# Kernel tuning notes

Hardware: AMD Instinct MI355X
Metric: run time of the kernel (lower is better)

The kernel has to match this reference:

```python
import jax, jax.numpy as jnp
import numpy as np

B, S, L = 8, 2048, 8
H, NH = 768, 12
DH = H // NH
NUM_REL = 100
LN_EPS = 1e-5


def setup_inputs() -> dict:
    key = jax.random.key(0)
    ks = jax.random.split(key, 16)
    inp = {
        'text_embeddings': jax.random.normal(ks[0], (B, S, H), dtype=jnp.float32),
        # values in [-1, 64); -1 marks 'no leaf' and is masked out
        'graph_structure': jax.random.randint(ks[1], (B, S, L), -1, 64, dtype=jnp.int64),
        'relation_ids': jax.random.randint(ks[2], (B, S, L), 0, NUM_REL, dtype=jnp.int64),
        'rel_table': jax.random.normal(ks[3], (NUM_REL, H), dtype=jnp.float32),
        'Wq': jax.random.normal(ks[4], (H, H), dtype=jnp.float32) / np.sqrt(H),
        'bq': jnp.zeros((H,), dtype=jnp.float32),
        'Wk': jax.random.normal(ks[5], (H, H), dtype=jnp.float32) / np.sqrt(H),
        'bk': jnp.zeros((H,), dtype=jnp.float32),
        'Wv': jax.random.normal(ks[6], (H, H), dtype=jnp.float32) / np.sqrt(H),
        'bv': jnp.zeros((H,), dtype=jnp.float32),
        'Wo': jax.random.normal(ks[7], (H, H), dtype=jnp.float32) / np.sqrt(H),
        'bo': jnp.zeros((H,), dtype=jnp.float32),
        'gamma': jnp.ones((H,), dtype=jnp.float32),
        'beta': jnp.zeros((H,), dtype=jnp.float32),
    }
    return inp


def reference(text_embeddings, graph_structure, relation_ids, rel_table,
              Wq, bq, Wk, bk, Wv, bv, Wo, bo, gamma, beta):
    b, s, h = text_embeddings.shape
    l = relation_ids.shape[2]
    # embedding gather (clamp -1 -> 0, masked later)
    rel_emb = rel_table[jnp.clip(relation_ids, 0, None)]  # [B,S,L,H]
    # projections; query has length-1 per root token
    q = (text_embeddings @ Wq + bq).reshape(b, s, NH, DH)          # [B,S,N,D]
    k = (rel_emb @ Wk + bk).reshape(b, s, l, NH, DH)               # [B,S,L,N,D]
    v = (rel_emb @ Wv + bv).reshape(b, s, l, NH, DH)
    scores = jnp.einsum('bsnd,bslnd->bsnl', q, k) / np.sqrt(DH)    # [B,S,N,L]
    mask = (graph_structure != -1)[:, :, None, :]                  # [B,S,1,L]
    scores = jnp.where(mask, scores, jnp.float32(-10000.0))
    probs = jax.nn.softmax(scores, axis=-1)                        # [B,S,N,L]
    ctx = jnp.einsum('bsnl,bslnd->bsnd', probs, v).reshape(b, s, h)
    out = ctx @ Wo + bo
    x = text_embeddings + out
    mu = jnp.mean(x, axis=-1, keepdims=True)
    var = jnp.mean(jnp.square(x - mu), axis=-1, keepdims=True)
    return (x - mu) * jax.lax.rsqrt(var + LN_EPS) * gamma + beta
```

## Files before the change

### kernel.cpp

```cpp
#include <hip/hip_runtime.h>
#include <hip/hip_bf16.h>

#define H 768
#define NH 12
#define DH 64
#define LL 8
#define NTOK 16384
#define NREL 100
#define NRELP 128
#define PADW 72

typedef __attribute__((ext_vector_type(8))) short short8;
typedef __attribute__((ext_vector_type(4))) float f32x4;

__device__ __forceinline__ float bf2f(ushort u) {
  union { unsigned int i; float f; } v; v.i = ((unsigned int)u) << 16; return v.f;
}
__device__ __forceinline__ float bflo(unsigned int u) {
  union { unsigned int i; float f; } v; v.i = u << 16; return v.f;
}
__device__ __forceinline__ float bfhi(unsigned int u) {
  union { unsigned int i; float f; } v; v.i = u & 0xffff0000u; return v.f;
}
__device__ __forceinline__ ushort f2bf(float f) {
  union { float f; unsigned int i; } v; v.f = f;
  unsigned int x = v.i;
  return (ushort)((x + 0x7fffu + ((x >> 16) & 1u)) >> 16);
}

#define NBX 12288
#define NBR 96
__global__ __launch_bounds__(256) void cvt_all_kernel(
    const float* __restrict__ X, ushort* __restrict__ Xbf,
    const float* __restrict__ rel, ushort* __restrict__ RelB) {
  int b = blockIdx.x;
  if (b < NBX) {
    int i = (b * 256 + threadIdx.x) * 4;
    float4 v = *(const float4*)(X + i);
    ushort4 o; o.x = f2bf(v.x); o.y = f2bf(v.y); o.z = f2bf(v.z); o.w = f2bf(v.w);
    *(ushort4*)(Xbf + i) = o;
  } else {
    int i = ((b - NBX) * 256 + threadIdx.x) * 4;
    int row = i / H;
    ushort4 o = {0, 0, 0, 0};
    if (row < NREL) {
      float4 v = *(const float4*)(rel + i);
      o.x = f2bf(v.x); o.y = f2bf(v.y); o.z = f2bf(v.z); o.w = f2bf(v.w);
    }
    *(ushort4*)(RelB + i) = o;
  }
}

__global__ __launch_bounds__(256) void transpose4_kernel(
    const float* __restrict__ s0, ushort* __restrict__ d0,
    const float* __restrict__ s1, ushort* __restrict__ d1,
    const float* __restrict__ s2, ushort* __restrict__ d2,
    const float* __restrict__ s3, ushort* __restrict__ d3) {
  const float* src; ushort* dst;
  switch (blockIdx.z) {
    case 0:  src = s0; dst = d0; break;
    case 1:  src = s1; dst = d1; break;
    case 2:  src = s2; dst = d2; break;
    default: src = s3; dst = d3; break;
  }
  __shared__ float tile[32][33];
  int bx = blockIdx.x * 32, by = blockIdx.y * 32;
  int tx = threadIdx.x & 31, ty = threadIdx.x >> 5;
  #pragma unroll
  for (int i = 0; i < 32; i += 8)
    tile[ty + i][tx] = src[(size_t)(by + ty + i) * H + bx + tx];
  __syncthreads();
  #pragma unroll
  for (int i = 0; i < 32; i += 8)
    dst[(size_t)(bx + ty + i) * H + by + tx] = f2bf(tile[tx][ty + i]);
}

__device__ __forceinline__ void gload_lds16(const void* g, void* l) {
  __builtin_amdgcn_global_load_lds(
      (const __attribute__((address_space(1))) unsigned int*)g,
      (__attribute__((address_space(3))) unsigned int*)l, 16, 0, 0);
}

#define BM 128
#define BN 128
#define BK 64

__device__ __forceinline__ void gemm_body(
    const ushort* __restrict__ A,
    const ushort* __restrict__ Bt,
    const float* __restrict__ bias,
    ushort* __restrict__ C,
    int M, int N, int K, int bx, int by) {
  __shared__ ushort As[BM * BK];
  __shared__ ushort Bs[BN * BK];
  const int tid = threadIdx.x;
  const int row0 = by * BM;
  const int col0 = bx * BN;
  const int wave = tid >> 6;
  const int lane = tid & 63;
  const int wr = wave >> 1, wc = wave & 1;
  const int lr = lane & 15, lk = lane >> 4;
  f32x4 acc[4][4];
  #pragma unroll
  for (int m = 0; m < 4; ++m)
    #pragma unroll
    for (int n = 0; n < 4; ++n) acc[m][n] = (f32x4)(0.f);

  for (int k0 = 0; k0 < K; k0 += BK) {
    #pragma unroll
    for (int i = 0; i < 4; ++i) {
      int c = tid + i * 256;
      int r = c >> 3, s = c & 7;
      int gs = s ^ (r & 7);
      gload_lds16(A  + (size_t)(row0 + r) * K + k0 + gs * 8, (char*)As + c * 16);
      gload_lds16(Bt + (size_t)(col0 + r) * K + k0 + gs * 8, (char*)Bs + c * 16);
    }
    __syncthreads();
    #pragma unroll
    for (int kk = 0; kk < 2; ++kk) {
      const int sw = (((kk << 2) | lk) ^ (lr & 7)) * 8;
      short8 af[4], bfr[4];
      #pragma unroll
      for (int m = 0; m < 4; ++m)
        af[m] = *(const short8*)(As + (wr * 64 + m * 16 + lr) * BK + sw);
      #pragma unroll
      for (int n = 0; n < 4; ++n)
        bfr[n] = *(const short8*)(Bs + (wc * 64 + n * 16 + lr) * BK + sw);
      #pragma unroll
      for (int m = 0; m < 4; ++m)
        #pragma unroll
        for (int n = 0; n < 4; ++n)
          acc[m][n] = __builtin_amdgcn_mfma_f32_16x16x32_bf16(af[m], bfr[n], acc[m][n], 0, 0, 0);
    }
    __syncthreads();
  }
  #pragma unroll
  for (int m = 0; m < 4; ++m) {
    #pragma unroll
    for (int n = 0; n < 4; ++n) {
      int col = col0 + wc * 64 + n * 16 + lr;
      float b = bias[col];
      #pragma unroll
      for (int j = 0; j < 4; ++j) {
        int row = row0 + wr * 64 + m * 16 + lk * 4 + j;
        C[(size_t)row * N + col] = f2bf(acc[m][n][j] + b);
      }
    }
  }
}

__global__ __launch_bounds__(256, 2) void gemm_bt_kernel(
    const ushort* __restrict__ A, const ushort* __restrict__ Bt,
    const float* __restrict__ bias, ushort* __restrict__ C,
    int M, int N, int K) {
  int lin = blockIdx.y * gridDim.x + blockIdx.x;
  int q = (gridDim.x * gridDim.y) >> 3;
  int wg = (lin & 7) * q + (lin >> 3);
  gemm_body(A, Bt, bias, C, M, N, K, wg % gridDim.x, wg / gridDim.x);
}

__global__ __launch_bounds__(256, 2) void gemm_kv_kernel(
    const ushort* __restrict__ A,
    const ushort* __restrict__ BtK, const float* __restrict__ bK, ushort* __restrict__ CK,
    const ushort* __restrict__ BtV, const float* __restrict__ bV, ushort* __restrict__ CV) {
  if (blockIdx.z == 0)
    gemm_body(A, BtK, bK, CK, NRELP, H, H, blockIdx.x, blockIdx.y);
  else
    gemm_body(A, BtV, bV, CV, NRELP, H, H, blockIdx.x, blockIdx.y);
}

__global__ __launch_bounds__(256) void attn3_kernel(
    const ushort* __restrict__ Q,
    const ushort* __restrict__ Ktab,
    const ushort* __restrict__ Vtab,
    const int* __restrict__ graph,
    const int* __restrict__ relid,
    ushort* __restrict__ Ctx) {
  __shared__ __align__(16) ushort Ks[NREL * PADW];
  __shared__ __align__(16) ushort Vs[NREL * PADW];
  const int tid = threadIdx.x;
  const int head = blockIdx.y;
  const int t = blockIdx.x * 256 + tid;

  #pragma unroll
  for (int i = 0; i < 4; ++i) {
    int c = tid + i * 256;
    if (c < NREL * 9) {
      int row = c / 9, slot = c - row * 9;
      int gs = (slot < 8) ? slot * 8 : 0;
      const size_t src = (size_t)row * H + head * DH + gs;
      gload_lds16(Ktab + src, (char*)Ks + (size_t)c * 16);
      gload_lds16(Vtab + src, (char*)Vs + (size_t)c * 16);
    }
  }

  const uint4* qp = (const uint4*)(Q + (size_t)t * H + head * DH);
  uint4 qw[8];
  #pragma unroll
  for (int j = 0; j < 8; ++j) qw[j] = qp[j];
  const int4* gp = (const int4*)(graph + (size_t)t * LL);
  const int4* rp = (const int4*)(relid + (size_t)t * LL);
  int4 ga = gp[0], gb = gp[1];
  int4 ra = rp[0], rb = rp[1];
  int gs[8] = {ga.x, ga.y, ga.z, ga.w, gb.x, gb.y, gb.z, gb.w};
  int rid[8] = {ra.x, ra.y, ra.z, ra.w, rb.x, rb.y, rb.z, rb.w};
  int koff[8];
  #pragma unroll
  for (int l = 0; l < 8; ++l) {
    int r = rid[l] < 0 ? 0 : rid[l];
    koff[l] = r * (PADW * 2);
  }

  __syncthreads();

  float s[8];
  #pragma unroll
  for (int l = 0; l < 8; ++l) s[l] = 0.f;
  #pragma unroll
  for (int j = 0; j < 8; ++j) {
    float qf[8];
    qf[0] = bflo(qw[j].x); qf[1] = bfhi(qw[j].x);
    qf[2] = bflo(qw[j].y); qf[3] = bfhi(qw[j].y);
    qf[4] = bflo(qw[j].z); qf[5] = bfhi(qw[j].z);
    qf[6] = bflo(qw[j].w); qf[7] = bfhi(qw[j].w);
    #pragma unroll
    for (int l = 0; l < 8; ++l) {
      uint4 kw = *(const uint4*)((const char*)Ks + koff[l] + j * 16);
      s[l] += qf[0] * bflo(kw.x) + qf[1] * bfhi(kw.x)
            + qf[2] * bflo(kw.y) + qf[3] * bfhi(kw.y)
            + qf[4] * bflo(kw.z) + qf[5] * bfhi(kw.z)
            + qf[6] * bflo(kw.w) + qf[7] * bfhi(kw.w);
    }
  }

  #pragma unroll
  for (int l = 0; l < 8; ++l)
    s[l] = (gs[l] != -1) ? s[l] * 0.125f : -10000.0f;
  float mx = s[0];
  #pragma unroll
  for (int l = 1; l < 8; ++l) mx = fmaxf(mx, s[l]);
  float p[8], den = 0.f;
  #pragma unroll
  for (int l = 0; l < 8; ++l) { p[l] = __expf(s[l] - mx); den += p[l]; }
  float inv = 1.f / den;
  #pragma unroll
  for (int l = 0; l < 8; ++l) p[l] *= inv;

  ushort* cp = Ctx + (size_t)t * H + head * DH;
  #pragma unroll
  for (int j = 0; j < 8; ++j) {
    float a[8];
    #pragma unroll
    for (int d = 0; d < 8; ++d) a[d] = 0.f;
    #pragma unroll
    for (int l = 0; l < 8; ++l) {
      uint4 vw = *(const uint4*)((const char*)Vs + koff[l] + j * 16);
      a[0] += p[l] * bflo(vw.x); a[1] += p[l] * bfhi(vw.x);
      a[2] += p[l] * bflo(vw.y); a[3] += p[l] * bfhi(vw.y);
      a[4] += p[l] * bflo(vw.z); a[5] += p[l] * bfhi(vw.z);
      a[6] += p[l] * bflo(vw.w); a[7] += p[l] * bfhi(vw.w);
    }
    short8 o;
    #pragma unroll
    for (int d = 0; d < 8; ++d) o[d] = (short)f2bf(a[d]);
    *(short8*)(cp + j * 8) = o;
  }
}

__global__ __launch_bounds__(192) void ln_kernel(
    const float* __restrict__ text, const ushort* __restrict__ op,
    const float* __restrict__ gamma, const float* __restrict__ beta,
    float* __restrict__ out) {
  int t = blockIdx.x;
  int c0 = threadIdx.x * 4;
  float4 tv = *(const float4*)(text + (size_t)t * H + c0);
  ushort4 ov = *(const ushort4*)(op + (size_t)t * H + c0);
  float x0 = tv.x + bf2f(ov.x), x1 = tv.y + bf2f(ov.y);
  float x2 = tv.z + bf2f(ov.z), x3 = tv.w + bf2f(ov.w);
  float s = x0 + x1 + x2 + x3;
  float s2 = x0 * x0 + x1 * x1 + x2 * x2 + x3 * x3;
  #pragma unroll
  for (int off = 32; off > 0; off >>= 1) {
    s  += __shfl_xor(s, off, 64);
    s2 += __shfl_xor(s2, off, 64);
  }
  __shared__ float red[2][3];
  int wave = threadIdx.x >> 6, lane = threadIdx.x & 63;
  if (lane == 0) { red[0][wave] = s; red[1][wave] = s2; }
  __syncthreads();
  s  = red[0][0] + red[0][1] + red[0][2];
  s2 = red[1][0] + red[1][1] + red[1][2];
  float mu = s * (1.f / H);
  float var = s2 * (1.f / H) - mu * mu;
  float rs = rsqrtf(var + 1e-5f);
  float4 g4 = *(const float4*)(gamma + c0);
  float4 b4 = *(const float4*)(beta + c0);
  float4 o4;
  o4.x = (x0 - mu) * rs * g4.x + b4.x;
  o4.y = (x1 - mu) * rs * g4.y + b4.y;
  o4.z = (x2 - mu) * rs * g4.z + b4.z;
  o4.w = (x3 - mu) * rs * g4.w + b4.w;
  *(float4*)(out + (size_t)t * H + c0) = o4;
}

extern "C" void kernel_launch(void* const* d_in, const int* in_sizes, int n_in,
                              void* d_out, int out_size, void* d_ws, size_t ws_size,
                              hipStream_t stream) {
  const float* text      = (const float*)d_in[0];
  const int*   graph     = (const int*)d_in[1];
  const int*   relid     = (const int*)d_in[2];
  const float* rel_table = (const float*)d_in[3];
  const float* Wq = (const float*)d_in[4];  const float* bq = (const float*)d_in[5];
  const float* Wk = (const float*)d_in[6];  const float* bk = (const float*)d_in[7];
  const float* Wv = (const float*)d_in[8];  const float* bv = (const float*)d_in[9];
  const float* Wo = (const float*)d_in[10]; const float* bo = (const float*)d_in[11];
  const float* gamma = (const float*)d_in[12];
  const float* beta  = (const float*)d_in[13];
  float* out = (float*)d_out;
  char* ws = (char*)d_ws;

  const size_t TOKH = (size_t)NTOK * H;
  size_t off = 0;
  ushort* Xbf  = (ushort*)(ws + off); off += TOKH * 2;
  ushort* Qbf  = (ushort*)(ws + off); off += TOKH * 2;
  ushort* WqT  = (ushort*)(ws + off); off += (size_t)H * H * 2;
  ushort* WoT  = (ushort*)(ws + off); off += (size_t)H * H * 2;
  ushort* WkT  = (ushort*)(ws + off); off += (size_t)H * H * 2;
  ushort* WvT  = (ushort*)(ws + off); off += (size_t)H * H * 2;
  ushort* RelB = (ushort*)(ws + off); off += (size_t)NRELP * H * 2;
  ushort* Ktab = (ushort*)(ws + off); off += (size_t)NRELP * H * 2;
  ushort* Vtab = (ushort*)(ws + off); off += (size_t)NRELP * H * 2;

  cvt_all_kernel<<<NBX + NBR, 256, 0, stream>>>(text, Xbf, rel_table, RelB);
  transpose4_kernel<<<dim3(H / 32, H / 32, 4), 256, 0, stream>>>(
      Wq, WqT, Wo, WoT, Wk, WkT, Wv, WvT);
  gemm_kv_kernel<<<dim3(H / BN, NRELP / BM, 2), 256, 0, stream>>>(
      RelB, WkT, bk, Ktab, WvT, bv, Vtab);
  dim3 g1(H / BN, NTOK / BM);
  gemm_bt_kernel<<<g1, 256, 0, stream>>>(Xbf, WqT, bq, Qbf, NTOK, H, H);
  dim3 ga(NTOK / 256, NH);
  attn3_kernel<<<ga, 256, 0, stream>>>(Qbf, Ktab, Vtab, graph, relid, Xbf);
  gemm_bt_kernel<<<g1, 256, 0, stream>>>(Xbf, WoT, bo, Qbf, NTOK, H, H);
  ln_kernel<<<NTOK, 192, 0, stream>>>(text, Qbf, gamma, beta, out);
}
```

Measured before the change: 124.0 us.

## Fuse fp32-to-bf16 conversion into Q GEMM and merge prep launches

```diff
diff --git a/kernel.cpp b/kernel.cpp
--- a/kernel.cpp
+++ b/kernel.cpp
@@ -27,35 +27,32 @@
   unsigned int x = v.i;
   return (ushort)((x + 0x7fffu + ((x >> 16) & 1u)) >> 16);
 }
-
-#define NBX 12288
-#define NBR 96
-__global__ __launch_bounds__(256) void cvt_all_kernel(
-    const float* __restrict__ X, ushort* __restrict__ Xbf,
-    const float* __restrict__ rel, ushort* __restrict__ RelB) {
-  int b = blockIdx.x;
-  if (b < NBX) {
-    int i = (b * 256 + threadIdx.x) * 4;
-    float4 v = *(const float4*)(X + i);
-    ushort4 o; o.x = f2bf(v.x); o.y = f2bf(v.y); o.z = f2bf(v.z); o.w = f2bf(v.w);
-    *(ushort4*)(Xbf + i) = o;
-  } else {
-    int i = ((b - NBX) * 256 + threadIdx.x) * 4;
-    int row = i / H;
-    ushort4 o = {0, 0, 0, 0};
-    if (row < NREL) {
-      float4 v = *(const float4*)(rel + i);
-      o.x = f2bf(v.x); o.y = f2bf(v.y); o.z = f2bf(v.z); o.w = f2bf(v.w);
-    }
-    *(ushort4*)(RelB + i) = o;
-  }
-}
-
-__global__ __launch_bounds__(256) void transpose4_kernel(
+__device__ __forceinline__ unsigned int cvt_pk_bf16(float lo, float hi) {
+  unsigned int r;
+  asm("v_cvt_pk_bf16_f32 %0, %1, %2" : "=v"(r) : "v"(lo), "v"(hi));
+  return r;
+}
+
+__global__ __launch_bounds__(256) void prep_kernel(
     const float* __restrict__ s0, ushort* __restrict__ d0,
     const float* __restrict__ s1, ushort* __restrict__ d1,
     const float* __restrict__ s2, ushort* __restrict__ d2,
-    const float* __restrict__ s3, ushort* __restrict__ d3) {
+    const float* __restrict__ s3, ushort* __restrict__ d3,
+    const float* __restrict__ rel, ushort* __restrict__ RelB) {
+  if (blockIdx.z == 4) {
+    int b = blockIdx.y * 24 + blockIdx.x;
+    if (b < 96) {
+      int i = (b * 256 + threadIdx.x) * 4;
+      int row = i / H;
+      ushort4 o = {0, 0, 0, 0};
+      if (row < NREL) {
+        float4 v = *(const float4*)(rel + i);
+        o.x = f2bf(v.x); o.y = f2bf(v.y); o.z = f2bf(v.z); o.w = f2bf(v.w);
+      }
+      *(ushort4*)(RelB + i) = o;
+    }
+    return;
+  }
   const float* src; ushort* dst;
   switch (blockIdx.z) {
     case 0:  src = s0; dst = d0; break;
@@ -85,14 +82,34 @@
 #define BN 128
 #define BK 64
 
+#define GEMM_COMPUTE_EPILOGUE()                                                \
+  __syncthreads();                                                             \
+  _Pragma("unroll")                                                            \
+  for (int kk = 0; kk < 2; ++kk) {                                             \
+    const int sw = (((kk << 2) | lk) ^ (lr & 7)) * 8;                          \
+    short8 af[4], bfr[4];                                                      \
+    _Pragma("unroll")                                                          \
+    for (int m = 0; m < 4; ++m)                                                \
+      af[m] = *(const short8*)(As + (wr * 64 + m * 16 + lr) * BK + sw);        \
+    _Pragma("unroll")                                                          \
+    for (int n = 0; n < 4; ++n)                                                \
+      bfr[n] = *(const short8*)(Bs + (wc * 64 + n * 16 + lr) * BK + sw);       \
+    _Pragma("unroll")                                                          \
+    for (int m = 0; m < 4; ++m)                                                \
+      _Pragma("unroll")                                                        \
+      for (int n = 0; n < 4; ++n)                                              \
+        acc[m][n] = __builtin_amdgcn_mfma_f32_16x16x32_bf16(af[m], bfr[n],     \
+                                                            acc[m][n], 0, 0, 0);\
+  }                                                                            \
+  __syncthreads();
+
 __device__ __forceinline__ void gemm_body(
+    ushort* As, ushort* Bs,
     const ushort* __restrict__ A,
     const ushort* __restrict__ Bt,
     const float* __restrict__ bias,
     ushort* __restrict__ C,
     int M, int N, int K, int bx, int by) {
-  __shared__ ushort As[BM * BK];
-  __shared__ ushort Bs[BN * BK];
   const int tid = threadIdx.x;
   const int row0 = by * BM;
   const int col0 = bx * BN;
@@ -115,24 +132,7 @@
       gload_lds16(A  + (size_t)(row0 + r) * K + k0 + gs * 8, (char*)As + c * 16);
       gload_lds16(Bt + (size_t)(col0 + r) * K + k0 + gs * 8, (char*)Bs + c * 16);
     }
-    __syncthreads();
-    #pragma unroll
-    for (int kk = 0; kk < 2; ++kk) {
-      const int sw = (((kk << 2) | lk) ^ (lr & 7)) * 8;
-      short8 af[4], bfr[4];
-      #pragma unroll
-      for (int m = 0; m < 4; ++m)
-        af[m] = *(const short8*)(As + (wr * 64 + m * 16 + lr) * BK + sw);
-      #pragma unroll
-      for (int n = 0; n < 4; ++n)
-        bfr[n] = *(const short8*)(Bs + (wc * 64 + n * 16 + lr) * BK + sw);
-      #pragma unroll
-      for (int m = 0; m < 4; ++m)
-        #pragma unroll
-        for (int n = 0; n < 4; ++n)
-          acc[m][n] = __builtin_amdgcn_mfma_f32_16x16x32_bf16(af[m], bfr[n], acc[m][n], 0, 0, 0);
-    }
-    __syncthreads();
+    GEMM_COMPUTE_EPILOGUE()
   }
   #pragma unroll
   for (int m = 0; m < 4; ++m) {
@@ -149,24 +149,89 @@
   }
 }
 
+__device__ __forceinline__ void gemm_body_a32(
+    ushort* As, ushort* Bs,
+    const float* __restrict__ A32,
+    const ushort* __restrict__ Bt,
+    const float* __restrict__ bias,
+    ushort* __restrict__ C,
+    int M, int N, int K, int bx, int by) {
+  const int tid = threadIdx.x;
+  const int row0 = by * BM;
+  const int col0 = bx * BN;
+  const int wave = tid >> 6;
+  const int lane = tid & 63;
+  const int wr = wave >> 1, wc = wave & 1;
+  const int lr = lane & 15, lk = lane >> 4;
+  f32x4 acc[4][4];
+  #pragma unroll
+  for (int m = 0; m < 4; ++m)
+    #pragma unroll
+    for (int n = 0; n < 4; ++n) acc[m][n] = (f32x4)(0.f);
+
+  for (int k0 = 0; k0 < K; k0 += BK) {
+    #pragma unroll
+    for (int i = 0; i < 4; ++i) {
+      int c = tid + i * 256;
+      int r = c >> 3, s = c & 7;
+      int gs = s ^ (r & 7);
+      gload_lds16(Bt + (size_t)(col0 + r) * K + k0 + gs * 8, (char*)Bs + c * 16);
+      const float* src = A32 + (size_t)(row0 + r) * K + k0 + gs * 8;
+      float4 f0 = *(const float4*)(src);
+      float4 f1 = *(const float4*)(src + 4);
+      uint4 w;
+      w.x = cvt_pk_bf16(f0.x, f0.y);
+      w.y = cvt_pk_bf16(f0.z, f0.w);
+      w.z = cvt_pk_bf16(f1.x, f1.y);
+      w.w = cvt_pk_bf16(f1.z, f1.w);
+      *(uint4*)((char*)As + c * 16) = w;
+    }
+    GEMM_COMPUTE_EPILOGUE()
+  }
+  #pragma unroll
+  for (int m = 0; m < 4; ++m) {
+    #pragma unroll
+    for (int n = 0; n < 4; ++n) {
+      int col = col0 + wc * 64 + n * 16 + lr;
+      float b = bias[col];
+      #pragma unroll
+      for (int j = 0; j < 4; ++j) {
+        int row = row0 + wr * 64 + m * 16 + lk * 4 + j;
+        C[(size_t)row * N + col] = f2bf(acc[m][n][j] + b);
+      }
+    }
+  }
+}
+
+__global__ __launch_bounds__(256, 2) void gemm_q_kv_kernel(
+    const float* __restrict__ X, const ushort* __restrict__ WqT,
+    const float* __restrict__ bq, ushort* __restrict__ Qbf,
+    const ushort* __restrict__ RelB,
+    const ushort* __restrict__ WkT, const float* __restrict__ bk, ushort* __restrict__ Ktab,
+    const ushort* __restrict__ WvT, const float* __restrict__ bv, ushort* __restrict__ Vtab) {
+  __shared__ ushort As[BM * BK];
+  __shared__ ushort Bs[BN * BK];
+  int lin = blockIdx.x;
+  if (lin < 12) {
+    if (lin < 6) gemm_body(As, Bs, RelB, WkT, bk, Ktab, NRELP, H, H, lin, 0);
+    else         gemm_body(As, Bs, RelB, WvT, bv, Vtab, NRELP, H, H, lin - 6, 0);
+    return;
+  }
+  int l2 = lin - 12;
+  int wg = (l2 & 7) * 96 + (l2 >> 3);
+  gemm_body_a32(As, Bs, X, WqT, bq, Qbf, NTOK, H, H, wg % 6, wg / 6);
+}
+
 __global__ __launch_bounds__(256, 2) void gemm_bt_kernel(
     const ushort* __restrict__ A, const ushort* __restrict__ Bt,
     const float* __restrict__ bias, ushort* __restrict__ C,
     int M, int N, int K) {
+  __shared__ ushort As[BM * BK];
+  __shared__ ushort Bs[BN * BK];
   int lin = blockIdx.y * gridDim.x + blockIdx.x;
   int q = (gridDim.x * gridDim.y) >> 3;
   int wg = (lin & 7) * q + (lin >> 3);
-  gemm_body(A, Bt, bias, C, M, N, K, wg % gridDim.x, wg / gridDim.x);
-}
-
-__global__ __launch_bounds__(256, 2) void gemm_kv_kernel(
-    const ushort* __restrict__ A,
-    const ushort* __restrict__ BtK, const float* __restrict__ bK, ushort* __restrict__ CK,
-    const ushort* __restrict__ BtV, const float* __restrict__ bV, ushort* __restrict__ CV) {
-  if (blockIdx.z == 0)
-    gemm_body(A, BtK, bK, CK, NRELP, H, H, blockIdx.x, blockIdx.y);
-  else
-    gemm_body(A, BtV, bV, CV, NRELP, H, H, blockIdx.x, blockIdx.y);
+  gemm_body(As, Bs, A, Bt, bias, C, M, N, K, wg % gridDim.x, wg / gridDim.x);
 }
 
 __global__ __launch_bounds__(256) void attn3_kernel(
@@ -321,7 +386,7 @@
 
   const size_t TOKH = (size_t)NTOK * H;
   size_t off = 0;
-  ushort* Xbf  = (ushort*)(ws + off); off += TOKH * 2;
+  ushort* Ctx  = (ushort*)(ws + off); off += TOKH * 2;
   ushort* Qbf  = (ushort*)(ws + off); off += TOKH * 2;
   ushort* WqT  = (ushort*)(ws + off); off += (size_t)H * H * 2;
   ushort* WoT  = (ushort*)(ws + off); off += (size_t)H * H * 2;
@@ -331,15 +396,13 @@
   ushort* Ktab = (ushort*)(ws + off); off += (size_t)NRELP * H * 2;
   ushort* Vtab = (ushort*)(ws + off); off += (size_t)NRELP * H * 2;
 
-  cvt_all_kernel<<<NBX + NBR, 256, 0, stream>>>(text, Xbf, rel_table, RelB);
-  transpose4_kernel<<<dim3(H / 32, H / 32, 4), 256, 0, stream>>>(
-      Wq, WqT, Wo, WoT, Wk, WkT, Wv, WvT);
-  gemm_kv_kernel<<<dim3(H / BN, NRELP / BM, 2), 256, 0, stream>>>(
-      RelB, WkT, bk, Ktab, WvT, bv, Vtab);
+  prep_kernel<<<dim3(24, 24, 5), 256, 0, stream>>>(
+      Wq, WqT, Wo, WoT, Wk, WkT, Wv, WvT, rel_table, RelB);
+  gemm_q_kv_kernel<<<780, 256, 0, stream>>>(
+      text, WqT, bq, Qbf, RelB, WkT, bk, Ktab, WvT, bv, Vtab);
+  dim3 ga(NTOK / 256, NH);
+  attn3_kernel<<<ga, 256, 0, stream>>>(Qbf, Ktab, Vtab, graph, relid, Ctx);
   dim3 g1(H / BN, NTOK / BM);
-  gemm_bt_kernel<<<g1, 256, 0, stream>>>(Xbf, WqT, bq, Qbf, NTOK, H, H);
-  dim3 ga(NTOK / 256, NH);
-  attn3_kernel<<<ga, 256, 0, stream>>>(Qbf, Ktab, Vtab, graph, relid, Xbf);
-  gemm_bt_kernel<<<g1, 256, 0, stream>>>(Xbf, WoT, bo, Qbf, NTOK, H, H);
+  gemm_bt_kernel<<<g1, 256, 0, stream>>>(Ctx, WoT, bo, Qbf, NTOK, H, H);
   ln_kernel<<<NTOK, 192, 0, stream>>>(text, Qbf, gamma, beta, out);
 }
```

Result: faster. 109.7 us (-11.5%).
